# Performance work log

Measured on AMD Instinct MI355X. Metric: run time of the kernel, lower is better.

## Reference

```python
import jax, jax.numpy as jnp
import numpy as np
from jax import lax

FIRE_RATE = 0.5
RNG_BASE = jax.random.key(42)


def _max_pool3(x):
    # 3x3 max pool, stride 1, SAME padding, over NCHW channel slice
    return lax.reduce_window(x, -jnp.inf, lax.max, (1, 1, 3, 3), (1, 1, 1, 1), 'SAME')


def _depthwise(x, k):
    c = x.shape[1]
    return lax.conv_general_dilated(
        x, k, window_strides=(1, 1), padding='SAME',
        feature_group_count=c, dimension_numbers=('NCHW', 'OIHW', 'NCHW'))


def setup_inputs() -> dict:
    key = jax.random.key(0)
    k1, k2, k3, k4, k5 = jax.random.split(key, 5)
    B, C, H, W, HID = 8, 16, 96, 96, 128
    x = jax.random.normal(k1, (B, C, H, W), dtype=jnp.float32)
    w1 = jax.random.normal(k2, (HID, 3 * C), dtype=jnp.float32) * 0.1
    b1 = jax.random.normal(k3, (HID,), dtype=jnp.float32) * 0.1
    w2 = jax.random.normal(k4, (C, HID), dtype=jnp.float32) * 0.05
    b2 = jax.random.normal(k5, (C,), dtype=jnp.float32) * 0.05
    return {'x': x, 'w1': w1, 'b1': b1, 'w2': w2, 'b2': b2, 'steps': 16}


def reference(x, w1, b1, w2, b2, steps):
    C = x.shape[1]
    sobel_x = jnp.array([[-1., 0., 1.], [-2., 0., 2.], [-1., 0., 1.]], jnp.float32) / 8.0
    sobel_y = sobel_x.T
    kx = jnp.broadcast_to(sobel_x, (C, 1, 3, 3))
    ky = jnp.broadcast_to(sobel_y, (C, 1, 3, 3))

    def step_fn(xc, i):
        pre_life = _max_pool3(xc[:, 3:4]) > 0.1
        # perception: [x, grad_x, grad_y] along channels -> (B, 3C, H, W)
        p = jnp.concatenate([xc, _depthwise(xc, kx), _depthwise(xc, ky)], axis=1)
        y = jax.nn.relu(jnp.einsum('bchw,oc->bohw', p, w1) + b1[None, :, None, None])
        update = jnp.einsum('bhcw,oh->bocw'.replace('h', 'k'), y, w2) if False else \
            jnp.einsum('bkhw,ok->bohw', y, w2) + b2[None, :, None, None]
        key_i = jax.random.fold_in(RNG_BASE, i)
        fire = (jax.random.uniform(key_i, (xc.shape[0], 1, xc.shape[2], xc.shape[3]))
                < FIRE_RATE).astype(xc.dtype)
        xn = xc + update * fire
        post_life = _max_pool3(xn[:, 3:4]) > 0.1
        life = (pre_life & post_life).astype(xc.dtype)
        xn = jnp.clip(xn * life, -10.0, 10.0)
        return xn, None

    x_out, _ = lax.scan(step_fn, x, jnp.arange(steps))
    return x_out
```

## Files before the change

kernel.cpp:

```cpp
#include <hip/hip_runtime.h>
#include <stdint.h>

#define BB 8
#define CC 16
#define HH 96
#define WW 96
#define HID 128
#define HW (HH*WW)
#define CHW (CC*HW)
#define NPIX (BB*HW)
#define STEPS 16

typedef short s16x8 __attribute__((ext_vector_type(8)));
typedef float f32x4 __attribute__((ext_vector_type(4)));

__device__ __host__ inline unsigned short bf16rne(float x) {
  union { float f; uint32_t u; } v; v.f = x;
  return (unsigned short)((v.u + 0x7fffu + ((v.u >> 16) & 1u)) >> 16);
}
__device__ __host__ inline float bf16f(unsigned short h) {
  union { uint32_t u; float f; } v; v.u = ((uint32_t)h) << 16; return v.f;
}

__host__ __device__ inline void threefry2x32(uint32_t k0, uint32_t k1,
                                             uint32_t x0, uint32_t x1,
                                             uint32_t& o0, uint32_t& o1) {
  const uint32_t ks2 = k0 ^ k1 ^ 0x1BD11BDAu;
  uint32_t v0 = x0 + k0, v1 = x1 + k1;
#define RL(v, r) (((v) << (r)) | ((v) >> (32 - (r))))
#define RND(r) { v0 += v1; v1 = RL(v1, r); v1 ^= v0; }
  RND(13) RND(15) RND(26) RND(6)   v0 += k1;  v1 += ks2 + 1u;
  RND(17) RND(29) RND(16) RND(24)  v0 += ks2; v1 += k0 + 2u;
  RND(13) RND(15) RND(26) RND(6)   v0 += k0;  v1 += k1 + 3u;
  RND(17) RND(29) RND(16) RND(24)  v0 += k1;  v1 += ks2 + 4u;
  RND(13) RND(15) RND(26) RND(6)   v0 += ks2; v1 += k0 + 5u;
#undef RND
#undef RL
  o0 = v0; o1 = v1;
}

__device__ inline float fire_val(uint32_t ka, uint32_t kb, uint32_t j) {
  uint32_t r0, r1;
  threefry2x32(ka, kb, 0u, j, r0, r1);
  return ((r0 ^ r1) & 0x80000000u) ? 0.0f : 1.0f;
}

__global__ void prep_w(const float* __restrict__ w1, const float* __restrict__ b1,
                       const float* __restrict__ w2,
                       unsigned short* __restrict__ w1fh, unsigned short* __restrict__ w1fl,
                       unsigned short* __restrict__ w2fh, unsigned short* __restrict__ w2fl) {
  int i = blockIdx.x * 256 + threadIdx.x;
  if (i < HID * 64) {
    int m = i >> 6, kn = i & 63;
    int q = kn >> 4, mm = kn & 15;
    float x;
    if (mm < 12) {
      int cc = mm / 3, j = mm - cc * 3;
      x = w1[m * 48 + j * 16 + q + cc * 4];
    } else if (kn == 15) {
      x = b1[m];
    } else {
      x = 0.f;
    }
    int mq = m >> 5, mp = (m >> 4) & 1, lm = m & 15;
    int kg = kn >> 3, e = kn & 7, ks = kg >> 2, lg = kg & 3;
    int dst = ((((mq * 2 + mp) * 2 + ks) * 64) + lg * 16 + lm) * 8 + e;
    unsigned short hb = bf16rne(x);
    w1fh[dst] = hb; w1fl[dst] = bf16rne(x - bf16f(hb));
  } else if (i < HID * 64 + CC * HID) {
    int j = i - HID * 64;
    int m = j >> 7, k = j & 127;
    float x = w2[m * 128 + k];
    int kg = k >> 3, e = k & 7, ks = kg >> 2, lg = kg & 3;
    int dst = ((ks * 64) + lg * 16 + m) * 8 + e;
    unsigned short hb = bf16rne(x);
    w2fh[dst] = hb; w2fl[dst] = bf16rne(x - bf16f(hb));
  }
}

__global__ __launch_bounds__(256, 3) void ca_fused(
    const float* __restrict__ src, const float* __restrict__ plprev,
    const unsigned short* __restrict__ w1fh, const unsigned short* __restrict__ w1fl,
    const unsigned short* __restrict__ w2fh, const unsigned short* __restrict__ w2fl,
    const float* __restrict__ b2,
    float* __restrict__ rawout, float* __restrict__ plout,
    uint32_t ka, uint32_t kb, int apply_life)
{
  __shared__ __align__(16) unsigned char smem[46592];
  unsigned char* pfh   = smem;
  unsigned char* pfl   = smem + 8192;
  unsigned char* yfh   = smem;
  unsigned char* yfl   = smem + 16384;
  float* xt            = (float*)(smem + 32768);
  float* raw3          = (float*)(smem + 44288);
  float* life_l        = (float*)(smem + 45248);
  float* fire_lds      = (float*)(smem + 45968);

  const int tid  = threadIdx.x;
  const int lane = tid & 63;
  const int q    = __builtin_amdgcn_readfirstlane(tid >> 6);
  const int b    = blockIdx.x & 7;
  const int t    = blockIdx.x >> 3;
  const int h0   = (t / 6) * 8, w0 = (t % 6) * 16;
  const int lm   = lane & 15, lg = lane >> 4;

  s16x8 a1h[2][2], a1l[2][2];
#pragma unroll
  for (int mp = 0; mp < 2; ++mp)
#pragma unroll
    for (int ks = 0; ks < 2; ++ks) {
      const int off = ((((q * 2 + mp) * 2 + ks) * 64) + lane) * 8;
      a1h[mp][ks] = *reinterpret_cast<const s16x8*>(w1fh + off);
      a1l[mp][ks] = *reinterpret_cast<const s16x8*>(w1fl + off);
    }
  const f32x4 b2v = reinterpret_cast<const f32x4*>(b2)[lg];

  float r3v = 0.f;
  if (apply_life && tid < 240) {
    const int r = tid / 20, c = tid - r * 20;
    const int hh = h0 - 2 + r, ww = w0 - 2 + c;
    if (hh >= 0 && hh < HH && ww >= 0 && ww < WW)
      r3v = src[b * CHW + 3 * HW + hh * WW + ww];
  }
  float plv = 0.f;
  if (apply_life && tid < 180) {
    const int r = tid / 18, c = tid - r * 18;
    const int hh = h0 - 1 + r, ww = w0 - 1 + c;
    if (hh >= 0 && hh < HH && ww >= 0 && ww < WW)
      plv = plprev[b * HW + hh * WW + ww];
  }
  float xreg[12];
#pragma unroll
  for (int ii = 0; ii < 12; ++ii) {
    xreg[ii] = 0.f;
    const int idx = tid + ii * 256;
    if (idx < CC * 180) {
      const int ch = idx / 180, rc = idx - ch * 180;
      const int r = rc / 18, c = rc - r * 18;
      const int hh = h0 - 1 + r, ww = w0 - 1 + c;
      if (hh >= 0 && hh < HH && ww >= 0 && ww < WW)
        xreg[ii] = src[b * CHW + ch * HW + hh * WW + ww];
    }
  }

  if (apply_life) {
    if (tid < 240) raw3[tid] = r3v;
    __syncthreads();
    if (tid < 180) {
      const int r = tid / 18, c = tid - r * 18;
      float m = fmaxf(fmaxf(raw3[r * 20 + c],        raw3[r * 20 + c + 1]),
                      fmaxf(raw3[r * 20 + c + 2],    raw3[(r + 1) * 20 + c]));
      m = fmaxf(m, fmaxf(raw3[(r + 1) * 20 + c + 1], raw3[(r + 1) * 20 + c + 2]));
      m = fmaxf(m, fmaxf(raw3[(r + 2) * 20 + c],     raw3[(r + 2) * 20 + c + 1]));
      m = fmaxf(m, raw3[(r + 2) * 20 + c + 2]);
      life_l[tid] = ((m > 0.1f) && (plv > 0.1f)) ? 1.f : 0.f;
    }
    __syncthreads();
  }

#pragma unroll
  for (int ii = 0; ii < 12; ++ii) {
    const int idx = tid + ii * 256;
    if (idx < CC * 180) {
      const int ch = idx / 180, rc = idx - ch * 180;
      float v = xreg[ii];
      if (apply_life) {
        v *= life_l[rc];
        v = fminf(fmaxf(v, -10.f), 10.f);
      }
      xt[ch * 180 + rc] = v;
    }
  }
  __syncthreads();

  if (tid < 128) {
    const int py = tid >> 4, pxx = tid & 15;
    const float* x3 = xt + 3 * 180;
    const int base = py * 18 + pxx;
    float m = fmaxf(fmaxf(x3[base],      x3[base + 1]),
                    fmaxf(x3[base + 2],  x3[base + 18]));
    m = fmaxf(m, fmaxf(x3[base + 19], x3[base + 20]));
    m = fmaxf(m, fmaxf(x3[base + 36], x3[base + 37]));
    m = fmaxf(m, x3[base + 38]);
    plout[b * HW + (h0 + py) * WW + w0 + pxx] = m;
  } else {
    const int i = tid - 128;
    const int py = i >> 4, pxx = i & 15;
    fire_lds[i] = fire_val(ka, kb, (uint32_t)(b * HW + (h0 + py) * WW + w0 + pxx));
  }

#pragma unroll 1
  for (int hf = 0; hf < 2; ++hf) {
    {
      const int pp  = hf * 64 + lane;
      const int ctr = ((pp >> 4) + 1) * 18 + (pp & 15) + 1;
      float fv[12];
#pragma unroll
      for (int cc = 0; cc < 4; ++cc) {
        const int c = q + cc * 4;
        const float* xc = xt + c * 180;
        const float v00 = xc[ctr - 19], v01 = xc[ctr - 18], v02 = xc[ctr - 17];
        const float v10 = xc[ctr - 1],  v11 = xc[ctr],      v12 = xc[ctr + 1];
        const float v20 = xc[ctr + 17], v21 = xc[ctr + 18], v22 = xc[ctr + 19];
        fv[cc * 3 + 0] = v11;
        fv[cc * 3 + 1] = ((v02 - v00) + 2.f * (v12 - v10) + (v22 - v20)) * 0.125f;
        fv[cc * 3 + 2] = ((v20 - v00) + 2.f * (v21 - v01) + (v22 - v02)) * 0.125f;
      }
      s16x8 ph[2], pl[2];
#pragma unroll
      for (int u = 0; u < 2; ++u)
#pragma unroll
        for (int e = 0; e < 8; ++e) {
          const int m = u * 8 + e;
          if (m < 12) {
            const unsigned short hb = bf16rne(fv[m]);
            ph[u][e] = (short)hb;
            pl[u][e] = (short)bf16rne(fv[m] - bf16f(hb));
          } else if (m == 15) {
            ph[u][e] = (short)((q == 0) ? 0x3F80 : 0);
            pl[u][e] = 0;
          } else {
            ph[u][e] = 0; pl[u][e] = 0;
          }
        }
#pragma unroll
      for (int u = 0; u < 2; ++u) {
        const int kgw = 2 * q + u;
        const int un = kgw * 64 + ((lane + kgw) & 63);
        *reinterpret_cast<s16x8*>(pfh + un * 16) = ph[u];
        *reinterpret_cast<s16x8*>(pfl + un * 16) = pl[u];
      }
    }
    __syncthreads();

    const int opx = q * 16 + lm;
    const int pp2 = hf * 64 + opx;
    const int opy = pp2 >> 4, owx = pp2 & 15;
    const int octr = (1 + opy) * 18 + (1 + owx);
    float xcv[4];
#pragma unroll
    for (int r = 0; r < 4; ++r) xcv[r] = xt[(lg * 4 + r) * 180 + octr];

    f32x4 acc[2][4];
#pragma unroll
    for (int mp = 0; mp < 2; ++mp)
#pragma unroll
      for (int nt = 0; nt < 4; ++nt) acc[mp][nt] = (f32x4){0.f, 0.f, 0.f, 0.f};

#pragma unroll
    for (int nt = 0; nt < 4; ++nt) {
#pragma unroll
      for (int ks = 0; ks < 2; ++ks) {
        const int kg = ks * 4 + lg;
        const int un = kg * 64 + ((nt * 16 + lm + kg) & 63);
        const s16x8 bh = *reinterpret_cast<const s16x8*>(pfh + un * 16);
        const s16x8 bl = *reinterpret_cast<const s16x8*>(pfl + un * 16);
#pragma unroll
        for (int mp = 0; mp < 2; ++mp) {
          acc[mp][nt] = __builtin_amdgcn_mfma_f32_16x16x32_bf16(a1l[mp][ks], bh, acc[mp][nt], 0, 0, 0);
          acc[mp][nt] = __builtin_amdgcn_mfma_f32_16x16x32_bf16(a1h[mp][ks], bl, acc[mp][nt], 0, 0, 0);
          acc[mp][nt] = __builtin_amdgcn_mfma_f32_16x16x32_bf16(a1h[mp][ks], bh, acc[mp][nt], 0, 0, 0);
        }
      }
    }
    __syncthreads();

#pragma unroll
    for (int mp = 0; mp < 2; ++mp) {
      const int k0 = (2 * q + mp) * 16 + lg * 4;
      const int kg = k0 >> 3, e0 = k0 & 7;
#pragma unroll
      for (int nt = 0; nt < 4; ++nt) {
        const int un = kg * 64 + ((nt * 16 + lm + kg) & 63);
        unsigned int hwv[2], lwv[2];
#pragma unroll
        for (int pr = 0; pr < 2; ++pr) {
          const float ya = fmaxf(acc[mp][nt][2 * pr], 0.f);
          const float yb = fmaxf(acc[mp][nt][2 * pr + 1], 0.f);
          const unsigned short ha = bf16rne(ya), hb2 = bf16rne(yb);
          const unsigned short la = bf16rne(ya - bf16f(ha));
          const unsigned short lb = bf16rne(yb - bf16f(hb2));
          hwv[pr] = (unsigned int)ha | ((unsigned int)hb2 << 16);
          lwv[pr] = (unsigned int)la | ((unsigned int)lb << 16);
        }
        *reinterpret_cast<uint2*>(yfh + un * 16 + e0 * 2) = make_uint2(hwv[0], hwv[1]);
        *reinterpret_cast<uint2*>(yfl + un * 16 + e0 * 2) = make_uint2(lwv[0], lwv[1]);
      }
    }
    __syncthreads();

    f32x4 acc2 = (f32x4){0.f, 0.f, 0.f, 0.f};
#pragma unroll
    for (int ks = 0; ks < 4; ++ks) {
      const int woff = ((ks * 64) + lane) * 8;
      const s16x8 a2l = *reinterpret_cast<const s16x8*>(w2fl + woff);
      const s16x8 a2h = *reinterpret_cast<const s16x8*>(w2fh + woff);
      const int kg = ks * 4 + lg;
      const int un = kg * 64 + ((q * 16 + lm + kg) & 63);
      const s16x8 bh = *reinterpret_cast<const s16x8*>(yfh + un * 16);
      const s16x8 bl = *reinterpret_cast<const s16x8*>(yfl + un * 16);
      acc2 = __builtin_amdgcn_mfma_f32_16x16x32_bf16(a2l, bh, acc2, 0, 0, 0);
      acc2 = __builtin_amdgcn_mfma_f32_16x16x32_bf16(a2h, bl, acc2, 0, 0, 0);
      acc2 = __builtin_amdgcn_mfma_f32_16x16x32_bf16(a2h, bh, acc2, 0, 0, 0);
    }

    const float fire = fire_lds[pp2];
    const int gb = b * CHW + (h0 + opy) * WW + (w0 + owx);
#pragma unroll
    for (int r = 0; r < 4; ++r) {
      const int c = lg * 4 + r;
      rawout[gb + c * HW] = xcv[r] + (acc2[r] + b2v[r]) * fire;
    }
    if (hf == 0) __syncthreads();
  }
}

__global__ __launch_bounds__(256) void ca_life(
    const float* __restrict__ prelife, const float* __restrict__ raw,
    float* __restrict__ xnext)
{
  const int lane = threadIdx.x & 63;
  const int g    = threadIdx.x >> 6;
  const int b    = blockIdx.x & 7;
  const int seg  = blockIdx.x >> 3;
  const int rem  = seg * 64 + lane;
  const int h = rem / WW;
  const int w = rem - h * WW;
  const int P = b * HW + rem;
  const bool hm = (h > 0), hp = (h < HH - 1), wm = (w > 0), wp = (w < WW - 1);

  float m2;
  {
    const float* xr = raw + b * CHW + 3 * HW + h * WW + w;
    m2 = xr[0];
    if (hm) {
      m2 = fmaxf(m2, xr[-WW]);
      if (wm) m2 = fmaxf(m2, xr[-WW - 1]);
      if (wp) m2 = fmaxf(m2, xr[-WW + 1]);
    }
    if (wm) m2 = fmaxf(m2, xr[-1]);
    if (wp) m2 = fmaxf(m2, xr[ 1]);
    if (hp) {
      m2 = fmaxf(m2, xr[WW]);
      if (wm) m2 = fmaxf(m2, xr[WW - 1]);
      if (wp) m2 = fmaxf(m2, xr[WW + 1]);
    }
  }
  const float life = ((prelife[P] > 0.1f) && (m2 > 0.1f)) ? 1.f : 0.f;

  const int base = b * CHW + h * WW + w;
#pragma unroll
  for (int cc = 0; cc < 4; ++cc) {
    const int c = g + cc * 4;
    float v = raw[base + c * HW] * life;
    v = fminf(fmaxf(v, -10.f), 10.f);
    xnext[base + c * HW] = v;
  }
}

extern "C" void kernel_launch(void* const* d_in, const int* in_sizes, int n_in,
                              void* d_out, int out_size, void* d_ws, size_t ws_size,
                              hipStream_t stream) {
  const float* x  = (const float*)d_in[0];
  const float* w1 = (const float*)d_in[1];
  const float* b1 = (const float*)d_in[2];
  const float* w2 = (const float*)d_in[3];
  const float* b2 = (const float*)d_in[4];
  float* out = (float*)d_out;

  char* ws = (char*)d_ws;
  const size_t BUF = (size_t)NPIX * CC * sizeof(float);
  float* rawA = (float*)(ws);
  float* rawB = (float*)(ws + BUF);
  float* plA  = (float*)(ws + 2 * BUF);
  float* plB  = (float*)(ws + 2 * BUF + (size_t)NPIX * 4);
  unsigned short* w1fh = (unsigned short*)(ws + 2 * BUF + 2 * (size_t)NPIX * 4);
  unsigned short* w1fl = w1fh + HID * 64;
  unsigned short* w2fh = w1fl + HID * 64;
  unsigned short* w2fl = w2fh + CC * HID;

  hipLaunchKernelGGL(prep_w, dim3(40), dim3(256), 0, stream,
                     w1, b1, w2, w1fh, w1fl, w2fh, w2fl);

  for (int i = 0; i < STEPS; ++i) {
    uint32_t ka, kb;
    threefry2x32(0u, 42u, 0u, (uint32_t)i, ka, kb);
    const float* src = (i == 0) ? x : ((i & 1) ? rawA : rawB);
    const float* plp = (i & 1) ? plA : plB;
    float* ro        = (i & 1) ? rawB : rawA;
    float* po        = (i & 1) ? plB : plA;
    hipLaunchKernelGGL(ca_fused, dim3(8 * 72), dim3(256), 0, stream,
                       src, plp, w1fh, w1fl, w2fh, w2fl, b2, ro, po,
                       ka, kb, (i == 0) ? 0 : 1);
  }
  hipLaunchKernelGGL(ca_life, dim3(NPIX / 64), dim3(256), 0, stream,
                     plB, rawB, out);
  (void)in_sizes; (void)n_in; (void)out_size; (void)ws_size;
}
```

Baseline: 228.0 us.

## Fuse all CA steps into one persistent kernel with neighbor-flag synchronization

Replaces the per-step kernel launches and the separate final life kernel with a single persistent kernel. Each block loops over all steps and waits only on its 8 neighboring tiles' progress flags, using agent-scope acquire and release atomics, before reading halo data. The final life mask and clamp are applied inside the same kernel. The intent is to remove launch gaps and grid-wide barriers between steps. The cost is spin-wait overhead, a flag memset, and a dependence on all 576 blocks being co-resident to avoid deadlock.

```diff
diff --git a/kernel.cpp b/kernel.cpp
--- a/kernel.cpp
+++ b/kernel.cpp
@@ -10,9 +10,12 @@
 #define CHW (CC*HW)
 #define NPIX (BB*HW)
 #define STEPS 16
+#define NBLK (8*72)
 
 typedef short s16x8 __attribute__((ext_vector_type(8)));
 typedef float f32x4 __attribute__((ext_vector_type(4)));
+
+struct KeyArr { uint32_t k[2 * STEPS]; };
 
 __device__ __host__ inline unsigned short bf16rne(float x) {
   union { float f; uint32_t u; } v; v.f = x;
@@ -78,13 +81,14 @@
   }
 }
 
-__global__ __launch_bounds__(256, 3) void ca_fused(
-    const float* __restrict__ src, const float* __restrict__ plprev,
+__global__ __launch_bounds__(256, 3) void ca_persist(
+    const float* __restrict__ x,
     const unsigned short* __restrict__ w1fh, const unsigned short* __restrict__ w1fl,
     const unsigned short* __restrict__ w2fh, const unsigned short* __restrict__ w2fl,
     const float* __restrict__ b2,
-    float* __restrict__ rawout, float* __restrict__ plout,
-    uint32_t ka, uint32_t kb, int apply_life)
+    float* __restrict__ rawA, float* __restrict__ rawB,
+    float* __restrict__ plA,  float* __restrict__ plB,
+    uint32_t* __restrict__ flags, KeyArr keys, float* __restrict__ out)
 {
   __shared__ __align__(16) unsigned char smem[46592];
   unsigned char* pfh   = smem;
@@ -104,6 +108,17 @@
   const int h0   = (t / 6) * 8, w0 = (t % 6) * 16;
   const int lm   = lane & 15, lg = lane >> 4;
 
+  bool nbv = false; int nbid = 0;
+  if (q == 0 && lane < 8) {
+    const int th = t / 6, tw = t % 6;
+    const int dy = (lane < 3) ? -1 : (lane < 5 ? 0 : 1);
+    const int dx = (lane == 0 || lane == 3 || lane == 5) ? -1
+                 : ((lane == 1 || lane == 6) ? 0 : 1);
+    const int ny = th + dy, nx = tw + dx;
+    nbv  = (ny >= 0 && ny < 12 && nx >= 0 && nx < 6);
+    nbid = b + 8 * (ny * 6 + nx);
+  }
+
   s16x8 a1h[2][2], a1l[2][2];
 #pragma unroll
   for (int mp = 0; mp < 2; ++mp)
@@ -115,246 +130,275 @@
     }
   const f32x4 b2v = reinterpret_cast<const f32x4*>(b2)[lg];
 
-  float r3v = 0.f;
-  if (apply_life && tid < 240) {
-    const int r = tid / 20, c = tid - r * 20;
-    const int hh = h0 - 2 + r, ww = w0 - 2 + c;
-    if (hh >= 0 && hh < HH && ww >= 0 && ww < WW)
-      r3v = src[b * CHW + 3 * HW + hh * WW + ww];
-  }
-  float plv = 0.f;
-  if (apply_life && tid < 180) {
-    const int r = tid / 18, c = tid - r * 18;
-    const int hh = h0 - 1 + r, ww = w0 - 1 + c;
-    if (hh >= 0 && hh < HH && ww >= 0 && ww < WW)
-      plv = plprev[b * HW + hh * WW + ww];
-  }
-  float xreg[12];
-#pragma unroll
-  for (int ii = 0; ii < 12; ++ii) {
-    xreg[ii] = 0.f;
-    const int idx = tid + ii * 256;
-    if (idx < CC * 180) {
-      const int ch = idx / 180, rc = idx - ch * 180;
-      const int r = rc / 18, c = rc - r * 18;
+#pragma unroll 1
+  for (int i = 0; i < STEPS; ++i) {
+    if (i > 0) {
+      if (q == 0 && lane < 8 && nbv) {
+        const uint32_t want = (uint32_t)i;
+        while (__hip_atomic_load(flags + nbid, __ATOMIC_RELAXED,
+                                 __HIP_MEMORY_SCOPE_AGENT) < want)
+          __builtin_amdgcn_s_sleep(8);
+        (void)__hip_atomic_load(flags + nbid, __ATOMIC_ACQUIRE,
+                                __HIP_MEMORY_SCOPE_AGENT);
+      }
+      __syncthreads();
+    }
+
+    const int apply_life = (i != 0);
+    const float* src = (i == 0) ? x : ((i & 1) ? rawA : rawB);
+    const float* plprev = (i & 1) ? plA : plB;
+    float* rawout = (i & 1) ? rawB : rawA;
+    float* plout  = (i & 1) ? plB : plA;
+    const uint32_t ka = keys.k[2 * i], kb = keys.k[2 * i + 1];
+
+    float r3v = 0.f;
+    if (apply_life && tid < 240) {
+      const int r = tid / 20, c = tid - r * 20;
+      const int hh = h0 - 2 + r, ww = w0 - 2 + c;
+      if (hh >= 0 && hh < HH && ww >= 0 && ww < WW)
+        r3v = src[b * CHW + 3 * HW + hh * WW + ww];
+    }
+    float plv = 0.f;
+    if (apply_life && tid < 180) {
+      const int r = tid / 18, c = tid - r * 18;
       const int hh = h0 - 1 + r, ww = w0 - 1 + c;
       if (hh >= 0 && hh < HH && ww >= 0 && ww < WW)
-        xreg[ii] = src[b * CHW + ch * HW + hh * WW + ww];
-    }
+        plv = plprev[b * HW + hh * WW + ww];
+    }
+    float xreg[12];
+#pragma unroll
+    for (int ii = 0; ii < 12; ++ii) {
+      xreg[ii] = 0.f;
+      const int idx = tid + ii * 256;
+      if (idx < CC * 180) {
+        const int ch = idx / 180, rc = idx - ch * 180;
+        const int r = rc / 18, c = rc - r * 18;
+        const int hh = h0 - 1 + r, ww = w0 - 1 + c;
+        if (hh >= 0 && hh < HH && ww >= 0 && ww < WW)
+          xreg[ii] = src[b * CHW + ch * HW + hh * WW + ww];
+      }
+    }
+
+    if (apply_life) {
+      if (tid < 240) raw3[tid] = r3v;
+      __syncthreads();
+      if (tid < 180) {
+        const int r = tid / 18, c = tid - r * 18;
+        float m = fmaxf(fmaxf(raw3[r * 20 + c],        raw3[r * 20 + c + 1]),
+                        fmaxf(raw3[r * 20 + c + 2],    raw3[(r + 1) * 20 + c]));
+        m = fmaxf(m, fmaxf(raw3[(r + 1) * 20 + c + 1], raw3[(r + 1) * 20 + c + 2]));
+        m = fmaxf(m, fmaxf(raw3[(r + 2) * 20 + c],     raw3[(r + 2) * 20 + c + 1]));
+        m = fmaxf(m, raw3[(r + 2) * 20 + c + 2]);
+        life_l[tid] = ((m > 0.1f) && (plv > 0.1f)) ? 1.f : 0.f;
+      }
+      __syncthreads();
+    }
+
+#pragma unroll
+    for (int ii = 0; ii < 12; ++ii) {
+      const int idx = tid + ii * 256;
+      if (idx < CC * 180) {
+        const int ch = idx / 180, rc = idx - ch * 180;
+        float v = xreg[ii];
+        if (apply_life) {
+          v *= life_l[rc];
+          v = fminf(fmaxf(v, -10.f), 10.f);
+        }
+        xt[ch * 180 + rc] = v;
+      }
+    }
+    __syncthreads();
+
+    if (tid < 128) {
+      const int py = tid >> 4, pxx = tid & 15;
+      const float* x3 = xt + 3 * 180;
+      const int base = py * 18 + pxx;
+      float m = fmaxf(fmaxf(x3[base],      x3[base + 1]),
+                      fmaxf(x3[base + 2],  x3[base + 18]));
+      m = fmaxf(m, fmaxf(x3[base + 19], x3[base + 20]));
+      m = fmaxf(m, fmaxf(x3[base + 36], x3[base + 37]));
+      m = fmaxf(m, x3[base + 38]);
+      plout[b * HW + (h0 + py) * WW + w0 + pxx] = m;
+    } else {
+      const int ii = tid - 128;
+      const int py = ii >> 4, pxx = ii & 15;
+      fire_lds[ii] = fire_val(ka, kb, (uint32_t)(b * HW + (h0 + py) * WW + w0 + pxx));
+    }
+
+#pragma unroll 1
+    for (int hf = 0; hf < 2; ++hf) {
+      {
+        const int pp  = hf * 64 + lane;
+        const int ctr = ((pp >> 4) + 1) * 18 + (pp & 15) + 1;
+        float fv[12];
+#pragma unroll
+        for (int cc = 0; cc < 4; ++cc) {
+          const int c = q + cc * 4;
+          const float* xc = xt + c * 180;
+          const float v00 = xc[ctr - 19], v01 = xc[ctr - 18], v02 = xc[ctr - 17];
+          const float v10 = xc[ctr - 1],  v11 = xc[ctr],      v12 = xc[ctr + 1];
+          const float v20 = xc[ctr + 17], v21 = xc[ctr + 18], v22 = xc[ctr + 19];
+          fv[cc * 3 + 0] = v11;
+          fv[cc * 3 + 1] = ((v02 - v00) + 2.f * (v12 - v10) + (v22 - v20)) * 0.125f;
+          fv[cc * 3 + 2] = ((v20 - v00) + 2.f * (v21 - v01) + (v22 - v02)) * 0.125f;
+        }
+        s16x8 ph[2], pl[2];
+#pragma unroll
+        for (int u = 0; u < 2; ++u)
+#pragma unroll
+          for (int e = 0; e < 8; ++e) {
+            const int m = u * 8 + e;
+            if (m < 12) {
+              const unsigned short hb = bf16rne(fv[m]);
+              ph[u][e] = (short)hb;
+              pl[u][e] = (short)bf16rne(fv[m] - bf16f(hb));
+            } else if (m == 15) {
+              ph[u][e] = (short)((q == 0) ? 0x3F80 : 0);
+              pl[u][e] = 0;
+            } else {
+              ph[u][e] = 0; pl[u][e] = 0;
+            }
+          }
+#pragma unroll
+        for (int u = 0; u < 2; ++u) {
+          const int kgw = 2 * q + u;
+          const int un = kgw * 64 + ((lane + kgw) & 63);
+          *reinterpret_cast<s16x8*>(pfh + un * 16) = ph[u];
+          *reinterpret_cast<s16x8*>(pfl + un * 16) = pl[u];
+        }
+      }
+      __syncthreads();
+
+      const int opx = q * 16 + lm;
+      const int pp2 = hf * 64 + opx;
+      const int opy = pp2 >> 4, owx = pp2 & 15;
+      const int octr = (1 + opy) * 18 + (1 + owx);
+      float xcv[4];
+#pragma unroll
+      for (int r = 0; r < 4; ++r) xcv[r] = xt[(lg * 4 + r) * 180 + octr];
+
+      f32x4 acc[2][4];
+#pragma unroll
+      for (int mp = 0; mp < 2; ++mp)
+#pragma unroll
+        for (int nt = 0; nt < 4; ++nt) acc[mp][nt] = (f32x4){0.f, 0.f, 0.f, 0.f};
+
+#pragma unroll
+      for (int nt = 0; nt < 4; ++nt) {
+#pragma unroll
+        for (int ks = 0; ks < 2; ++ks) {
+          const int kg = ks * 4 + lg;
+          const int un = kg * 64 + ((nt * 16 + lm + kg) & 63);
+          const s16x8 bh = *reinterpret_cast<const s16x8*>(pfh + un * 16);
+          const s16x8 bl = *reinterpret_cast<const s16x8*>(pfl + un * 16);
+#pragma unroll
+          for (int mp = 0; mp < 2; ++mp) {
+            acc[mp][nt] = __builtin_amdgcn_mfma_f32_16x16x32_bf16(a1l[mp][ks], bh, acc[mp][nt], 0, 0, 0);
+            acc[mp][nt] = __builtin_amdgcn_mfma_f32_16x16x32_bf16(a1h[mp][ks], bl, acc[mp][nt], 0, 0, 0);
+            acc[mp][nt] = __builtin_amdgcn_mfma_f32_16x16x32_bf16(a1h[mp][ks], bh, acc[mp][nt], 0, 0, 0);
+          }
+        }
+      }
+      __syncthreads();
+
+#pragma unroll
+      for (int mp = 0; mp < 2; ++mp) {
+        const int k0 = (2 * q + mp) * 16 + lg * 4;
+        const int kg = k0 >> 3, e0 = k0 & 7;
+#pragma unroll
+        for (int nt = 0; nt < 4; ++nt) {
+          const int un = kg * 64 + ((nt * 16 + lm + kg) & 63);
+          unsigned int hwv[2], lwv[2];
+#pragma unroll
+          for (int pr = 0; pr < 2; ++pr) {
+            const float ya = fmaxf(acc[mp][nt][2 * pr], 0.f);
+            const float yb = fmaxf(acc[mp][nt][2 * pr + 1], 0.f);
+            const unsigned short ha = bf16rne(ya), hb2 = bf16rne(yb);
+            const unsigned short la = bf16rne(ya - bf16f(ha));
+            const unsigned short lb = bf16rne(yb - bf16f(hb2));
+            hwv[pr] = (unsigned int)ha | ((unsigned int)hb2 << 16);
+            lwv[pr] = (unsigned int)la | ((unsigned int)lb << 16);
+          }
+          *reinterpret_cast<uint2*>(yfh + un * 16 + e0 * 2) = make_uint2(hwv[0], hwv[1]);
+          *reinterpret_cast<uint2*>(yfl + un * 16 + e0 * 2) = make_uint2(lwv[0], lwv[1]);
+        }
+      }
+      __syncthreads();
+
+      f32x4 acc2 = (f32x4){0.f, 0.f, 0.f, 0.f};
+#pragma unroll
+      for (int ks = 0; ks < 4; ++ks) {
+        const int woff = ((ks * 64) + lane) * 8;
+        const s16x8 a2l = *reinterpret_cast<const s16x8*>(w2fl + woff);
+        const s16x8 a2h = *reinterpret_cast<const s16x8*>(w2fh + woff);
+        const int kg = ks * 4 + lg;
+        const int un = kg * 64 + ((q * 16 + lm + kg) & 63);
+        const s16x8 bh = *reinterpret_cast<const s16x8*>(yfh + un * 16);
+        const s16x8 bl = *reinterpret_cast<const s16x8*>(yfl + un * 16);
+        acc2 = __builtin_amdgcn_mfma_f32_16x16x32_bf16(a2l, bh, acc2, 0, 0, 0);
+        acc2 = __builtin_amdgcn_mfma_f32_16x16x32_bf16(a2h, bl, acc2, 0, 0, 0);
+        acc2 = __builtin_amdgcn_mfma_f32_16x16x32_bf16(a2h, bh, acc2, 0, 0, 0);
+      }
+
+      const float fire = fire_lds[pp2];
+      const int gb = b * CHW + (h0 + opy) * WW + (w0 + owx);
+#pragma unroll
+      for (int r = 0; r < 4; ++r) {
+        const int c = lg * 4 + r;
+        rawout[gb + c * HW] = xcv[r] + (acc2[r] + b2v[r]) * fire;
+      }
+      if (hf == 0) __syncthreads();
+    }
+
+    __syncthreads();
+    if (tid == 0)
+      __hip_atomic_store(flags + blockIdx.x, (uint32_t)(i + 1),
+                         __ATOMIC_RELEASE, __HIP_MEMORY_SCOPE_AGENT);
   }
 
-  if (apply_life) {
-    if (tid < 240) raw3[tid] = r3v;
-    __syncthreads();
-    if (tid < 180) {
-      const int r = tid / 18, c = tid - r * 18;
-      float m = fmaxf(fmaxf(raw3[r * 20 + c],        raw3[r * 20 + c + 1]),
-                      fmaxf(raw3[r * 20 + c + 2],    raw3[(r + 1) * 20 + c]));
-      m = fmaxf(m, fmaxf(raw3[(r + 1) * 20 + c + 1], raw3[(r + 1) * 20 + c + 2]));
-      m = fmaxf(m, fmaxf(raw3[(r + 2) * 20 + c],     raw3[(r + 2) * 20 + c + 1]));
-      m = fmaxf(m, raw3[(r + 2) * 20 + c + 2]);
-      life_l[tid] = ((m > 0.1f) && (plv > 0.1f)) ? 1.f : 0.f;
-    }
-    __syncthreads();
-  }
-
-#pragma unroll
-  for (int ii = 0; ii < 12; ++ii) {
-    const int idx = tid + ii * 256;
-    if (idx < CC * 180) {
-      const int ch = idx / 180, rc = idx - ch * 180;
-      float v = xreg[ii];
-      if (apply_life) {
-        v *= life_l[rc];
-        v = fminf(fmaxf(v, -10.f), 10.f);
-      }
-      xt[ch * 180 + rc] = v;
-    }
+  if (q == 0 && lane < 8 && nbv) {
+    while (__hip_atomic_load(flags + nbid, __ATOMIC_RELAXED,
+                             __HIP_MEMORY_SCOPE_AGENT) < (uint32_t)STEPS)
+      __builtin_amdgcn_s_sleep(8);
+    (void)__hip_atomic_load(flags + nbid, __ATOMIC_ACQUIRE,
+                            __HIP_MEMORY_SCOPE_AGENT);
   }
   __syncthreads();
-
-  if (tid < 128) {
-    const int py = tid >> 4, pxx = tid & 15;
-    const float* x3 = xt + 3 * 180;
-    const int base = py * 18 + pxx;
-    float m = fmaxf(fmaxf(x3[base],      x3[base + 1]),
-                    fmaxf(x3[base + 2],  x3[base + 18]));
-    m = fmaxf(m, fmaxf(x3[base + 19], x3[base + 20]));
-    m = fmaxf(m, fmaxf(x3[base + 36], x3[base + 37]));
-    m = fmaxf(m, x3[base + 38]);
-    plout[b * HW + (h0 + py) * WW + w0 + pxx] = m;
-  } else {
-    const int i = tid - 128;
-    const int py = i >> 4, pxx = i & 15;
-    fire_lds[i] = fire_val(ka, kb, (uint32_t)(b * HW + (h0 + py) * WW + w0 + pxx));
-  }
-
-#pragma unroll 1
-  for (int hf = 0; hf < 2; ++hf) {
-    {
-      const int pp  = hf * 64 + lane;
-      const int ctr = ((pp >> 4) + 1) * 18 + (pp & 15) + 1;
-      float fv[12];
-#pragma unroll
-      for (int cc = 0; cc < 4; ++cc) {
-        const int c = q + cc * 4;
-        const float* xc = xt + c * 180;
-        const float v00 = xc[ctr - 19], v01 = xc[ctr - 18], v02 = xc[ctr - 17];
-        const float v10 = xc[ctr - 1],  v11 = xc[ctr],      v12 = xc[ctr + 1];
-        const float v20 = xc[ctr + 17], v21 = xc[ctr + 18], v22 = xc[ctr + 19];
-        fv[cc * 3 + 0] = v11;
-        fv[cc * 3 + 1] = ((v02 - v00) + 2.f * (v12 - v10) + (v22 - v20)) * 0.125f;
-        fv[cc * 3 + 2] = ((v20 - v00) + 2.f * (v21 - v01) + (v22 - v02)) * 0.125f;
-      }
-      s16x8 ph[2], pl[2];
-#pragma unroll
-      for (int u = 0; u < 2; ++u)
-#pragma unroll
-        for (int e = 0; e < 8; ++e) {
-          const int m = u * 8 + e;
-          if (m < 12) {
-            const unsigned short hb = bf16rne(fv[m]);
-            ph[u][e] = (short)hb;
-            pl[u][e] = (short)bf16rne(fv[m] - bf16f(hb));
-          } else if (m == 15) {
-            ph[u][e] = (short)((q == 0) ? 0x3F80 : 0);
-            pl[u][e] = 0;
-          } else {
-            ph[u][e] = 0; pl[u][e] = 0;
-          }
-        }
-#pragma unroll
-      for (int u = 0; u < 2; ++u) {
-        const int kgw = 2 * q + u;
-        const int un = kgw * 64 + ((lane + kgw) & 63);
-        *reinterpret_cast<s16x8*>(pfh + un * 16) = ph[u];
-        *reinterpret_cast<s16x8*>(pfl + un * 16) = pl[u];
-      }
+  {
+    float* life2 = life_l;
+    if (tid < 128) {
+      const int py = tid >> 4, pxx = tid & 15;
+      const int h = h0 + py, w = w0 + pxx;
+      const int P = b * HW + h * WW + w;
+      const bool hm = (h > 0), hp = (h < HH - 1), wm = (w > 0), wp = (w < WW - 1);
+      const float* xr = rawB + b * CHW + 3 * HW + h * WW + w;
+      float m2 = xr[0];
+      if (hm) {
+        m2 = fmaxf(m2, xr[-WW]);
+        if (wm) m2 = fmaxf(m2, xr[-WW - 1]);
+        if (wp) m2 = fmaxf(m2, xr[-WW + 1]);
+      }
+      if (wm) m2 = fmaxf(m2, xr[-1]);
+      if (wp) m2 = fmaxf(m2, xr[ 1]);
+      if (hp) {
+        m2 = fmaxf(m2, xr[WW]);
+        if (wm) m2 = fmaxf(m2, xr[WW - 1]);
+        if (wp) m2 = fmaxf(m2, xr[WW + 1]);
+      }
+      life2[tid] = ((plB[P] > 0.1f) && (m2 > 0.1f)) ? 1.f : 0.f;
     }
     __syncthreads();
-
-    const int opx = q * 16 + lm;
-    const int pp2 = hf * 64 + opx;
-    const int opy = pp2 >> 4, owx = pp2 & 15;
-    const int octr = (1 + opy) * 18 + (1 + owx);
-    float xcv[4];
-#pragma unroll
-    for (int r = 0; r < 4; ++r) xcv[r] = xt[(lg * 4 + r) * 180 + octr];
-
-    f32x4 acc[2][4];
-#pragma unroll
-    for (int mp = 0; mp < 2; ++mp)
-#pragma unroll
-      for (int nt = 0; nt < 4; ++nt) acc[mp][nt] = (f32x4){0.f, 0.f, 0.f, 0.f};
-
-#pragma unroll
-    for (int nt = 0; nt < 4; ++nt) {
-#pragma unroll
-      for (int ks = 0; ks < 2; ++ks) {
-        const int kg = ks * 4 + lg;
-        const int un = kg * 64 + ((nt * 16 + lm + kg) & 63);
-        const s16x8 bh = *reinterpret_cast<const s16x8*>(pfh + un * 16);
-        const s16x8 bl = *reinterpret_cast<const s16x8*>(pfl + un * 16);
-#pragma unroll
-        for (int mp = 0; mp < 2; ++mp) {
-          acc[mp][nt] = __builtin_amdgcn_mfma_f32_16x16x32_bf16(a1l[mp][ks], bh, acc[mp][nt], 0, 0, 0);
-          acc[mp][nt] = __builtin_amdgcn_mfma_f32_16x16x32_bf16(a1h[mp][ks], bl, acc[mp][nt], 0, 0, 0);
-          acc[mp][nt] = __builtin_amdgcn_mfma_f32_16x16x32_bf16(a1h[mp][ks], bh, acc[mp][nt], 0, 0, 0);
-        }
-      }
-    }
-    __syncthreads();
-
-#pragma unroll
-    for (int mp = 0; mp < 2; ++mp) {
-      const int k0 = (2 * q + mp) * 16 + lg * 4;
-      const int kg = k0 >> 3, e0 = k0 & 7;
-#pragma unroll
-      for (int nt = 0; nt < 4; ++nt) {
-        const int un = kg * 64 + ((nt * 16 + lm + kg) & 63);
-        unsigned int hwv[2], lwv[2];
-#pragma unroll
-        for (int pr = 0; pr < 2; ++pr) {
-          const float ya = fmaxf(acc[mp][nt][2 * pr], 0.f);
-          const float yb = fmaxf(acc[mp][nt][2 * pr + 1], 0.f);
-          const unsigned short ha = bf16rne(ya), hb2 = bf16rne(yb);
-          const unsigned short la = bf16rne(ya - bf16f(ha));
-          const unsigned short lb = bf16rne(yb - bf16f(hb2));
-          hwv[pr] = (unsigned int)ha | ((unsigned int)hb2 << 16);
-          lwv[pr] = (unsigned int)la | ((unsigned int)lb << 16);
-        }
-        *reinterpret_cast<uint2*>(yfh + un * 16 + e0 * 2) = make_uint2(hwv[0], hwv[1]);
-        *reinterpret_cast<uint2*>(yfl + un * 16 + e0 * 2) = make_uint2(lwv[0], lwv[1]);
-      }
-    }
-    __syncthreads();
-
-    f32x4 acc2 = (f32x4){0.f, 0.f, 0.f, 0.f};
-#pragma unroll
-    for (int ks = 0; ks < 4; ++ks) {
-      const int woff = ((ks * 64) + lane) * 8;
-      const s16x8 a2l = *reinterpret_cast<const s16x8*>(w2fl + woff);
-      const s16x8 a2h = *reinterpret_cast<const s16x8*>(w2fh + woff);
-      const int kg = ks * 4 + lg;
-      const int un = kg * 64 + ((q * 16 + lm + kg) & 63);
-      const s16x8 bh = *reinterpret_cast<const s16x8*>(yfh + un * 16);
-      const s16x8 bl = *reinterpret_cast<const s16x8*>(yfl + un * 16);
-      acc2 = __builtin_amdgcn_mfma_f32_16x16x32_bf16(a2l, bh, acc2, 0, 0, 0);
-      acc2 = __builtin_amdgcn_mfma_f32_16x16x32_bf16(a2h, bl, acc2, 0, 0, 0);
-      acc2 = __builtin_amdgcn_mfma_f32_16x16x32_bf16(a2h, bh, acc2, 0, 0, 0);
-    }
-
-    const float fire = fire_lds[pp2];
-    const int gb = b * CHW + (h0 + opy) * WW + (w0 + owx);
-#pragma unroll
-    for (int r = 0; r < 4; ++r) {
-      const int c = lg * 4 + r;
-      rawout[gb + c * HW] = xcv[r] + (acc2[r] + b2v[r]) * fire;
-    }
-    if (hf == 0) __syncthreads();
-  }
-}
-
-__global__ __launch_bounds__(256) void ca_life(
-    const float* __restrict__ prelife, const float* __restrict__ raw,
-    float* __restrict__ xnext)
-{
-  const int lane = threadIdx.x & 63;
-  const int g    = threadIdx.x >> 6;
-  const int b    = blockIdx.x & 7;
-  const int seg  = blockIdx.x >> 3;
-  const int rem  = seg * 64 + lane;
-  const int h = rem / WW;
-  const int w = rem - h * WW;
-  const int P = b * HW + rem;
-  const bool hm = (h > 0), hp = (h < HH - 1), wm = (w > 0), wp = (w < WW - 1);
-
-  float m2;
-  {
-    const float* xr = raw + b * CHW + 3 * HW + h * WW + w;
-    m2 = xr[0];
-    if (hm) {
-      m2 = fmaxf(m2, xr[-WW]);
-      if (wm) m2 = fmaxf(m2, xr[-WW - 1]);
-      if (wp) m2 = fmaxf(m2, xr[-WW + 1]);
-    }
-    if (wm) m2 = fmaxf(m2, xr[-1]);
-    if (wp) m2 = fmaxf(m2, xr[ 1]);
-    if (hp) {
-      m2 = fmaxf(m2, xr[WW]);
-      if (wm) m2 = fmaxf(m2, xr[WW - 1]);
-      if (wp) m2 = fmaxf(m2, xr[WW + 1]);
-    }
-  }
-  const float life = ((prelife[P] > 0.1f) && (m2 > 0.1f)) ? 1.f : 0.f;
-
-  const int base = b * CHW + h * WW + w;
-#pragma unroll
-  for (int cc = 0; cc < 4; ++cc) {
-    const int c = g + cc * 4;
-    float v = raw[base + c * HW] * life;
-    v = fminf(fmaxf(v, -10.f), 10.f);
-    xnext[base + c * HW] = v;
+    const int pxi = tid & 127, half = tid >> 7;
+    const int py = pxi >> 4, pxx = pxi & 15;
+    const int gb2 = b * CHW + (h0 + py) * WW + (w0 + pxx);
+    const float lf = life2[pxi];
+#pragma unroll
+    for (int cc = 0; cc < 8; ++cc) {
+      const int c = half * 8 + cc;
+      float v = rawB[gb2 + c * HW] * lf;
+      v = fminf(fmaxf(v, -10.f), 10.f);
+      out[gb2 + c * HW] = v;
+    }
   }
 }
 
@@ -378,22 +422,18 @@
   unsigned short* w1fl = w1fh + HID * 64;
   unsigned short* w2fh = w1fl + HID * 64;
   unsigned short* w2fl = w2fh + CC * HID;
+  uint32_t* flags = (uint32_t*)(w2fl + CC * HID);
 
   hipLaunchKernelGGL(prep_w, dim3(40), dim3(256), 0, stream,
                      w1, b1, w2, w1fh, w1fl, w2fh, w2fl);
-
-  for (int i = 0; i < STEPS; ++i) {
-    uint32_t ka, kb;
-    threefry2x32(0u, 42u, 0u, (uint32_t)i, ka, kb);
-    const float* src = (i == 0) ? x : ((i & 1) ? rawA : rawB);
-    const float* plp = (i & 1) ? plA : plB;
-    float* ro        = (i & 1) ? rawB : rawA;
-    float* po        = (i & 1) ? plB : plA;
-    hipLaunchKernelGGL(ca_fused, dim3(8 * 72), dim3(256), 0, stream,
-                       src, plp, w1fh, w1fl, w2fh, w2fl, b2, ro, po,
-                       ka, kb, (i == 0) ? 0 : 1);
-  }
-  hipLaunchKernelGGL(ca_life, dim3(NPIX / 64), dim3(256), 0, stream,
-                     plB, rawB, out);
+  hipMemsetAsync(flags, 0, NBLK * sizeof(uint32_t), stream);
+
+  KeyArr keys;
+  for (int i = 0; i < STEPS; ++i)
+    threefry2x32(0u, 42u, 0u, (uint32_t)i, keys.k[2 * i], keys.k[2 * i + 1]);
+
+  hipLaunchKernelGGL(ca_persist, dim3(NBLK), dim3(256), 0, stream,
+                     x, w1fh, w1fl, w2fh, w2fl, b2,
+                     rawA, rawB, plA, plB, flags, keys, out);
   (void)in_sizes; (void)n_in; (void)out_size; (void)ws_size;
 }
```

After: 456.0 us. 100.0% more time.
